# Performance work log

Hardware: AMD Instinct MI355X
Metric: run time of the kernel (lower is better)

## Reference

```python
import jax, jax.numpy as jnp
import numpy as np
from jax.scipy.special import digamma, gammaln

B, N, H, W, D = 16, 1024, 32, 32, 256
TEMP = 0.5
KL_WEIGHT = 1e-3


def setup_inputs() -> dict:
    key = jax.random.key(0)
    k1, k2, k3 = jax.random.split(key, 3)
    logits = jax.random.normal(k1, (B, N, H, W), dtype=jnp.float32)
    # codebook initialized uniform(-1/N, 1/N) as in init_type == 'uniform'
    codebook = jax.random.uniform(k2, (N, D), dtype=jnp.float32,
                                  minval=-1.0 / N, maxval=1.0 / N)
    # uniform noise for the Gumbel-softmax rsample (channels-last layout [B,H,W,N])
    uniform_noise = jax.random.uniform(k3, (B, H, W, N), dtype=jnp.float32,
                                       minval=1e-6, maxval=1.0 - 1e-6)
    return {"logits": logits, "codebook": codebook, "uniform_noise": uniform_noise}


def reference(logits, codebook, uniform_noise):
    # convert_to_alpha: evidential mapping alpha = softplus(logits) + 1,
    # then permute(0,2,3,1) -> [B, H, W, N]
    alpha = jax.nn.softplus(jnp.transpose(logits, (0, 2, 3, 1))) + 1.0
    S = jnp.sum(alpha, axis=-1, keepdims=True)            # [B,H,W,1]
    probs = alpha / S                                      # [B,H,W,N]

    # RelaxedOneHotCategorical(temp, probs).rsample() == Gumbel-softmax
    gumbel = -jnp.log(-jnp.log(uniform_noise))
    sample = jax.nn.softmax((jnp.log(probs) + gumbel) / TEMP, axis=-1)  # [B,H,W,N]

    vector_weights = jnp.transpose(sample, (0, 3, 1, 2))   # [B,N,H,W]
    indices = jnp.argmax(vector_weights, axis=1)           # [B,H,W]

    # quantized output via codebook combine
    z_q = jnp.einsum('bnhw,nd->bdhw', vector_weights, codebook)  # [B,D,H,W]

    # KL( Dirichlet(alpha) || Dirichlet(ones(N)) ), closed form with beta=1:
    # lgamma(S) - sum lgamma(alpha) - lgamma(N) + sum (alpha-1)*(digamma(alpha)-digamma(S))
    S1 = S[..., 0]
    kl = (gammaln(S1)
          - jnp.sum(gammaln(alpha), axis=-1)
          - gammaln(jnp.float32(N))
          + jnp.sum((alpha - 1.0) * (digamma(alpha) - digamma(S)), axis=-1))
    kl_loss = KL_WEIGHT * jnp.mean(kl)

    # perplexity over soft encodings
    avg_probs = jnp.mean(sample.reshape(-1, N), axis=0)
    perplexity = jnp.exp(-jnp.sum(avg_probs * jnp.log(avg_probs + 1e-10)))

    return (z_q, kl_loss, indices, perplexity)
```

## Files before the change

### kernel.cpp

```cpp
#include <hip/hip_runtime.h>
#include <math.h>

#define NB 16
#define NN 1024
#define NH 32
#define NW 32
#define ND 256
#define NPIX (NB*NH*NW)

#define ZQ_OFF  0
#define KL_OFF  4194304
#define IDX_OFF 4194305
#define PPL_OFF 4210689

#define LGAMMA_1024F 6071.2804f
#define BS_ROW_B 2080

typedef _Float16 f16x8 __attribute__((ext_vector_type(8)));
typedef _Float16 f16x4 __attribute__((ext_vector_type(4)));
typedef float    f32x4 __attribute__((ext_vector_type(4)));

__device__ __forceinline__ float fast_rcp(float x){ return __builtin_amdgcn_rcpf(x); }

__device__ __forceinline__ void lgamma_digamma(float a, float& lg, float& dg){
    float a1 = a + 1.f, a2 = a + 2.f, z = a + 3.f;
    float t12  = a1*a2;
    float prod = a*t12;
    float rz = fast_rcp(z);
    float rp = fast_rcp(prod);
    float lz = __logf(z);
    float lp = __logf(prod);
    float rz2 = rz*rz;
    lg = (z - 0.5f)*lz - z + 0.918938533f
       + rz*(0.083333333f - 0.002777778f*rz2) - lp;
    float sr = (t12 + a*(a + a + 3.f))*rp;
    dg = lz - 0.5f*rz - rz2*(0.083333333f - 0.008333333f*rz2) - sr;
}

__device__ __forceinline__ float elem(float x, float u,
                                      float& S, float& L, float& P){
    float t  = __expf(-fabsf(x));
    float a  = fmaxf(x, 0.f) + __logf(1.f + t) + 1.f;
    float lg, dg;
    lgamma_digamma(a, lg, dg);
    S += a; L += lg; P += (a - 1.f)*dg;
    float d = 1.f - u;
    float lup = -d*(1.f + d*(0.5f + d*(0.33333333f + d*(0.25f
              + d*(0.2f + d*(0.16666667f + d*0.14285714f))))));
    float lu = (d < 0.09f) ? lup : __logf(u);
    float ar = a * fast_rcp(lu);
    return ar*ar;
}

__global__ __launch_bounds__(256) void k_tr(
    const float* __restrict__ cb, _Float16* __restrict__ cbT)
{
    const int kb = blockIdx.x, kq = blockIdx.y, d = threadIdx.x;
    _Float16 tmp[8];
#pragma unroll
    for (int i = 0; i < 8; ++i)
        tmp[i] = (_Float16)cb[(size_t)(32*kb + 8*kq + i)*ND + d];
    *(f16x8*)(cbT + (size_t)kb*8192 + (size_t)d*32 + 8*kq) = *(f16x8*)tmp;
}

__global__ __launch_bounds__(1024, 2) void k_mega(
    const float* __restrict__ logits, const float* __restrict__ noise,
    const _Float16* __restrict__ cbT, float* __restrict__ colpart,
    float* __restrict__ klpart, float* __restrict__ out)
{
    __shared__ __align__(16) char lds[16*BS_ROW_B + 6*256*4];
    char*  bsb  = lds;
    float* redS = (float*)(lds + 16*BS_ROW_B);
    float* redL = redS + 256;
    float* redP = redL + 256;
    float* redZ = redP + 256;
    float* redM = redZ + 256;
    int*   redI = (int*)(redM + 256);

    const int t    = threadIdx.x;
    const int row  = blockIdx.x >> 1;
    const int w0   = (blockIdx.x & 1) * 16;
    const int b    = row >> 5, h = row & 31;
    const int lane = t & 63;
    const int v    = t >> 6;
    const int wl   = lane & 15;
    const int j4   = (lane >> 4) & 3;
    const int p    = row*32 + w0 + wl;
    const int nq   = 4*v + j4;

    const float* lgB = logits + (size_t)b*(NN*NH*NW) + (size_t)(4*nq)*(NH*NW)
                     + (size_t)h*NW + w0 + wl;
    const float* nzB = noise  + (size_t)p*NN + 4*nq;

    f32x4 u0, u1, u2, u3;
    float x00,x01,x02,x03, x10,x11,x12,x13;
    float x20,x21,x22,x23, x30,x31,x32,x33;
    float ev[16];
    float Sa = 0.f, La = 0.f, Pa = 0.f, Za = 0.f;
    float Sb = 0.f, Lb = 0.f, Pb = 0.f, Zb = 0.f;
    float mxA = -1.f, mxB = -1.f;
    int   idxA = 0, idxB = 0;

    asm volatile(
        "global_load_dwordx4 %0, %4, off\n\t"
        "global_load_dwordx4 %1, %4, off offset:1024\n\t"
        "global_load_dwordx4 %2, %4, off offset:2048\n\t"
        "global_load_dwordx4 %3, %4, off offset:3072"
        : "=&v"(u0), "=&v"(u1), "=&v"(u2), "=&v"(u3)
        : "v"(nzB));

#define LG_ASM(X0,X1,X2,X3,KK) \
    asm volatile( \
        "global_load_dword %0, %4, off offset:-4096\n\t" \
        "global_load_dword %1, %4, off\n\t" \
        "global_load_dword %2, %5, off offset:-4096\n\t" \
        "global_load_dword %3, %5, off" \
        : "=&v"(X0), "=&v"(X1), "=&v"(X2), "=&v"(X3) \
        : "v"(lgB + (size_t)(256*(KK))*1024 + 1024), \
          "v"(lgB + (size_t)(256*(KK))*1024 + 3072))

    LG_ASM(x00,x01,x02,x03, 0);
    LG_ASM(x10,x11,x12,x13, 1);
    LG_ASM(x20,x21,x22,x23, 2);
    LG_ASM(x30,x31,x32,x33, 3);
#undef LG_ASM

#define WAITV(NSTR) do{ asm volatile("s_waitcnt vmcnt(" NSTR ")"); \
                        __builtin_amdgcn_sched_barrier(0); }while(0)

#define DO_EA(kk,mm,X,UC) do{                                     \
    float e = elem(X, UC, Sa, La, Pa);                            \
    Za += e;                                                      \
    if (e > mxA){ mxA = e; idxA = 256*(kk) + 4*nq + (mm); }       \
    ev[4*(kk)+(mm)] = e; }while(0)

#define DO_EB(kk,mm,X,UC) do{                                     \
    float e = elem(X, UC, Sb, Lb, Pb);                            \
    Zb += e;                                                      \
    if (e > mxB){ mxB = e; idxB = 256*(kk) + 4*nq + (mm); }       \
    ev[4*(kk)+(mm)] = e; }while(0)

    WAITV("12");
    DO_EA(0,0,x00,u0[0]); DO_EB(0,1,x01,u0[1]);
    DO_EA(0,2,x02,u0[2]); DO_EB(0,3,x03,u0[3]);
    WAITV("8");
    DO_EA(1,0,x10,u1[0]); DO_EB(1,1,x11,u1[1]);
    DO_EA(1,2,x12,u1[2]); DO_EB(1,3,x13,u1[3]);
    WAITV("4");
    DO_EA(2,0,x20,u2[0]); DO_EB(2,1,x21,u2[1]);
    DO_EA(2,2,x22,u2[2]); DO_EB(2,3,x23,u2[3]);
    WAITV("0");
    DO_EA(3,0,x30,u3[0]); DO_EB(3,1,x31,u3[1]);
    DO_EA(3,2,x32,u3[2]); DO_EB(3,3,x33,u3[3]);
#undef WAITV
#undef DO_EA
#undef DO_EB

    float S = Sa + Sb, L = La + Lb, P = Pa + Pb, Z = Za + Zb;
    float mx; int idx;
    {
        bool take = (mxB > mxA) || (mxB == mxA && idxB < idxA);
        mx  = take ? mxB : mxA;
        idx = take ? idxB : idxA;
    }

#pragma unroll
    for (int mask = 16; mask < 64; mask <<= 1){
        S += __shfl_xor(S, mask);
        L += __shfl_xor(L, mask);
        P += __shfl_xor(P, mask);
        Z += __shfl_xor(Z, mask);
        float mo = __shfl_xor(mx, mask);
        int   io = __shfl_xor(idx, mask);
        bool take = (mo > mx) || (mo == mx && io < idx);
        mx  = take ? mo : mx;
        idx = take ? io : idx;
    }
    if (j4 == 0){
        redS[16*v + wl] = S;  redL[16*v + wl] = L;
        redP[16*v + wl] = P;  redZ[16*v + wl] = Z;
        redM[16*v + wl] = mx; redI[16*v + wl] = idx;
    }
    __syncthreads();

    float Zt = 0.f;
#pragma unroll
    for (int qz = 0; qz < 16; ++qz) Zt += redZ[16*qz + wl];
    const float zinv = fast_rcp(Zt);

    {
        char* brow = bsb + wl*BS_ROW_B;
        const int sw   = wl & 7;
        const int sub8 = (nq & 1) << 3;
        const int cb2  = nq >> 1;
#pragma unroll
        for (int k = 0; k < 4; ++k){
            f16x4 hv;
            hv[0] = (_Float16)(ev[4*k+0]*zinv);
            hv[1] = (_Float16)(ev[4*k+1]*zinv);
            hv[2] = (_Float16)(ev[4*k+2]*zinv);
            hv[3] = (_Float16)(ev[4*k+3]*zinv);
            *(f16x4*)(brow + (((32*k + cb2) ^ sw) << 4) + sub8) = hv;
        }
    }
    __syncthreads();

    const _Float16* aBase = cbT + (size_t)(16*v + wl)*32 + j4*8;
    const char* bRow = bsb + wl*BS_ROW_B;
    const int fsw = wl & 7;

    f32x4 acc = (f32x4)0.f;
    f16x8 ar[4];
    ar[0] = *(const f16x8*)(aBase);
    ar[1] = *(const f16x8*)(aBase + 8192);
    ar[2] = *(const f16x8*)(aBase + 2*8192);
    __builtin_amdgcn_sched_barrier(0);

#pragma unroll
    for (int kb = 0; kb < 32; ++kb){
        if (kb + 3 < 32){
            ar[(kb+3)&3] = *(const f16x8*)(aBase + (size_t)(kb+3)*8192);
            __builtin_amdgcn_sched_barrier(0);
        }
        f16x8 bf = *(const f16x8*)(bRow + ((((kb << 2) | j4) ^ fsw) << 4));
        acc = __builtin_amdgcn_mfma_f32_16x16x32_f16(ar[kb&3], bf, acc, 0, 0, 0);
    }

    float* outp = out + (size_t)b*(ND*1024) + h*32 + w0;
#pragma unroll
    for (int r = 0; r < 4; ++r){
        int d = 16*v + 4*j4 + r;
        outp[(size_t)d*1024 + wl] = acc[r];
    }

    {
        float s0 = 0.f;
#pragma unroll
        for (int r = 0; r < 16; ++r){
            const char* br = bsb + r*BS_ROW_B;
            const int sw2 = r & 7;
            s0 += (float)*(const _Float16*)(br + ((((t >> 3) ^ sw2) << 4) + 2*(t & 7)));
        }
        colpart[(size_t)blockIdx.x*NN + t] = s0;
    }

    if (t < 16){
        float Sq = 0.f, Lq = 0.f, Pq = 0.f, M = -1.f;
        int I = 0x7fffffff;
#pragma unroll
        for (int qz = 0; qz < 16; ++qz){
            Sq += redS[16*qz + t]; Lq += redL[16*qz + t]; Pq += redP[16*qz + t];
            float m = redM[16*qz + t]; int i = redI[16*qz + t];
            bool take = (m > M) || (m == M && i < I);
            M = take ? m : M; I = take ? i : I;
        }
        out[IDX_OFF + row*32 + w0 + t] = (float)I;
        float rS  = fast_rcp(Sq);
        float lnS = __logf(Sq);
        float lgS = (Sq - 0.5f)*lnS - Sq + 0.918938533f + 0.083333333f*rS;
        float dgS = lnS - 0.5f*rS;
        float kl = lgS - Lq - LGAMMA_1024F + (Pq - dgS*(Sq - 1024.f));
#pragma unroll
        for (int mask = 1; mask < 16; mask <<= 1) kl += __shfl_xor(kl, mask);
        if (t == 0) klpart[blockIdx.x] = kl;
    }
}

__global__ __launch_bounds__(256) void k_red(
    const float* __restrict__ colpart, float* __restrict__ colsum)
{
    __shared__ float red[8][32];
    const int nl = threadIdx.x & 31;
    const int rs = threadIdx.x >> 5;
    const int n  = blockIdx.x*32 + nl;
    const float* cp = colpart + (size_t)rs*128*NN + n;
    float s = 0.f;
#pragma unroll 8
    for (int r = 0; r < 128; ++r)
        s += cp[(size_t)r*NN];
    red[rs][nl] = s;
    __syncthreads();
    if (threadIdx.x < 32){
        float tot = 0.f;
#pragma unroll
        for (int i = 0; i < 8; ++i) tot += red[i][threadIdx.x];
        colsum[blockIdx.x*32 + threadIdx.x] = tot;
    }
}

__global__ __launch_bounds__(256) void k_final(
    const float* __restrict__ colsum, const float* __restrict__ klpart,
    float* __restrict__ out)
{
    __shared__ float red[8];
    const int tid = threadIdx.x;
    float s = 0.f, kls = 0.f;
#pragma unroll
    for (int n = tid; n < NN; n += 256){
        float avg = colsum[n] * (1.f/16384.f);
        s += avg * logf(avg + 1e-10f);
        kls += klpart[n];
    }
#pragma unroll
    for (int mask = 1; mask < 64; mask <<= 1){
        s   += __shfl_xor(s, mask);
        kls += __shfl_xor(kls, mask);
    }
    if ((tid & 63) == 0){ red[tid >> 6] = s; red[4 + (tid >> 6)] = kls; }
    __syncthreads();
    if (tid == 0){
        float tot = red[0] + red[1] + red[2] + red[3];
        float klt = red[4] + red[5] + red[6] + red[7];
        out[PPL_OFF] = expf(-tot);
        out[KL_OFF]  = 1e-3f * (klt * (1.f/16384.f));
    }
}

extern "C" void kernel_launch(void* const* d_in, const int* in_sizes, int n_in,
                              void* d_out, int out_size, void* d_ws, size_t ws_size,
                              hipStream_t stream)
{
    const float* logits = (const float*)d_in[0];
    const float* cb     = (const float*)d_in[1];
    const float* noise  = (const float*)d_in[2];
    float* out = (float*)d_out;

    float* colpart = (float*)d_ws;
    float* colsum  = colpart + (size_t)1024*NN;
    float* klpart  = colsum + NN;
    _Float16* cbT  = (_Float16*)(klpart + NN);

    k_tr   <<<dim3(32, 4), 256, 0, stream>>>(cb, cbT);
    k_mega <<<dim3(1024), 1024, 0, stream>>>(logits, noise, cbT, colpart, klpart, out);
    k_red  <<<dim3(32),    256, 0, stream>>>(colpart, colsum);
    k_final<<<1, 256, 0, stream>>>(colsum, klpart, out);
}
```

Measured before the change: 204.5 us.

## Pack element math into float2 vectors and defer lgamma product logs

Rewrites the per-element softplus/lgamma/digamma computation on two-wide float vectors so the compiler can emit packed FP32 instructions. It also drops the per-element log(prod) term from lgamma: the products are multiplied into running accumulators and a single log is taken per accumulator at the end. Separately, it removes the sched_barriers around the codebook prefetch in the MFMA loop, letting the compiler schedule loads freely. This trades transcendental work for a risk of overflow or precision loss when multiplying eight products of values up to around 3x, and it may change how well load latency is hidden.

```diff
diff --git a/kernel.cpp b/kernel.cpp
--- a/kernel.cpp
+++ b/kernel.cpp
@@ -19,36 +19,37 @@
 typedef _Float16 f16x8 __attribute__((ext_vector_type(8)));
 typedef _Float16 f16x4 __attribute__((ext_vector_type(4)));
 typedef float    f32x4 __attribute__((ext_vector_type(4)));
+typedef float    f32x2 __attribute__((ext_vector_type(2)));
 
 __device__ __forceinline__ float fast_rcp(float x){ return __builtin_amdgcn_rcpf(x); }
 
-__device__ __forceinline__ void lgamma_digamma(float a, float& lg, float& dg){
-    float a1 = a + 1.f, a2 = a + 2.f, z = a + 3.f;
-    float t12  = a1*a2;
-    float prod = a*t12;
-    float rz = fast_rcp(z);
-    float rp = fast_rcp(prod);
-    float lz = __logf(z);
-    float lp = __logf(prod);
-    float rz2 = rz*rz;
-    lg = (z - 0.5f)*lz - z + 0.918938533f
-       + rz*(0.083333333f - 0.002777778f*rz2) - lp;
-    float sr = (t12 + a*(a + a + 3.f))*rp;
-    dg = lz - 0.5f*rz - rz2*(0.083333333f - 0.008333333f*rz2) - sr;
-}
-
-__device__ __forceinline__ float elem(float x, float u,
-                                      float& S, float& L, float& P){
-    float t  = __expf(-fabsf(x));
-    float a  = fmaxf(x, 0.f) + __logf(1.f + t) + 1.f;
-    float lg, dg;
-    lgamma_digamma(a, lg, dg);
+__device__ __forceinline__ f32x2 elem2(f32x2 x, f32x2 u,
+                                       f32x2& S, f32x2& L, f32x2& P,
+                                       f32x2& prodAcc){
+    f32x2 t;   t[0] = __expf(-fabsf(x[0]));  t[1] = __expf(-fabsf(x[1]));
+    f32x2 mx0; mx0[0] = fmaxf(x[0], 0.f);    mx0[1] = fmaxf(x[1], 0.f);
+    f32x2 l1p; l1p[0] = __logf(1.f + t[0]);  l1p[1] = __logf(1.f + t[1]);
+    f32x2 a  = mx0 + l1p + 1.f;
+    f32x2 a1 = a + 1.f, a2 = a + 2.f, z = a + 3.f;
+    f32x2 t12  = a1*a2;
+    f32x2 prod = a*t12;
+    f32x2 rz;  rz[0] = fast_rcp(z[0]);       rz[1] = fast_rcp(z[1]);
+    f32x2 rp;  rp[0] = fast_rcp(prod[0]);    rp[1] = fast_rcp(prod[1]);
+    f32x2 lz;  lz[0] = __logf(z[0]);         lz[1] = __logf(z[1]);
+    prodAcc = prodAcc * prod;
+    f32x2 rz2 = rz*rz;
+    f32x2 lg = (z - 0.5f)*lz - z + 0.918938533f
+             + rz*(0.083333333f - 0.002777778f*rz2);
+    f32x2 sr = (t12 + a*(a + a + 3.f))*rp;
+    f32x2 dg = lz - 0.5f*rz - rz2*(0.083333333f - 0.008333333f*rz2) - sr;
     S += a; L += lg; P += (a - 1.f)*dg;
-    float d = 1.f - u;
-    float lup = -d*(1.f + d*(0.5f + d*(0.33333333f + d*(0.25f
+    f32x2 d = 1.f - u;
+    f32x2 lup = -d*(1.f + d*(0.5f + d*(0.33333333f + d*(0.25f
               + d*(0.2f + d*(0.16666667f + d*0.14285714f))))));
-    float lu = (d < 0.09f) ? lup : __logf(u);
-    float ar = a * fast_rcp(lu);
+    f32x2 lu;
+    lu[0] = (d[0] < 0.09f) ? lup[0] : __logf(u[0]);
+    lu[1] = (d[1] < 0.09f) ? lup[1] : __logf(u[1]);
+    f32x2 ar; ar[0] = a[0]*fast_rcp(lu[0]);  ar[1] = a[1]*fast_rcp(lu[1]);
     return ar*ar;
 }
 
@@ -96,8 +97,9 @@
     float x00,x01,x02,x03, x10,x11,x12,x13;
     float x20,x21,x22,x23, x30,x31,x32,x33;
     float ev[16];
-    float Sa = 0.f, La = 0.f, Pa = 0.f, Za = 0.f;
-    float Sb = 0.f, Lb = 0.f, Pb = 0.f, Zb = 0.f;
+    f32x2 SA = (f32x2)0.f, LA = (f32x2)0.f, PA = (f32x2)0.f, ZA = (f32x2)0.f;
+    f32x2 SB = (f32x2)0.f, LB = (f32x2)0.f, PB = (f32x2)0.f, ZB = (f32x2)0.f;
+    f32x2 prA = (f32x2)1.f, prB = (f32x2)1.f;
     float mxA = -1.f, mxB = -1.f;
     int   idxA = 0, idxB = 0;
 
@@ -128,35 +130,36 @@
 #define WAITV(NSTR) do{ asm volatile("s_waitcnt vmcnt(" NSTR ")"); \
                         __builtin_amdgcn_sched_barrier(0); }while(0)
 
-#define DO_EA(kk,mm,X,UC) do{                                     \
-    float e = elem(X, UC, Sa, La, Pa);                            \
-    Za += e;                                                      \
-    if (e > mxA){ mxA = e; idxA = 256*(kk) + 4*nq + (mm); }       \
-    ev[4*(kk)+(mm)] = e; }while(0)
-
-#define DO_EB(kk,mm,X,UC) do{                                     \
-    float e = elem(X, UC, Sb, Lb, Pb);                            \
-    Zb += e;                                                      \
-    if (e > mxB){ mxB = e; idxB = 256*(kk) + 4*nq + (mm); }       \
-    ev[4*(kk)+(mm)] = e; }while(0)
+#define DO_PAIR(kk, X0,X1,X2,X3, UV) do{                          \
+    f32x2 xA_, xB_, uA_, uB_;                                     \
+    xA_[0]=X0; xA_[1]=X1; xB_[0]=X2; xB_[1]=X3;                   \
+    uA_[0]=UV[0]; uA_[1]=UV[1]; uB_[0]=UV[2]; uB_[1]=UV[3];       \
+    f32x2 eA = elem2(xA_, uA_, SA, LA, PA, prA);                  \
+    f32x2 eB = elem2(xB_, uB_, SB, LB, PB, prB);                  \
+    ZA += eA; ZB += eB;                                           \
+    if (eA[0] > mxA){ mxA = eA[0]; idxA = 256*(kk) + 4*nq + 0; }  \
+    if (eA[1] > mxA){ mxA = eA[1]; idxA = 256*(kk) + 4*nq + 1; }  \
+    if (eB[0] > mxB){ mxB = eB[0]; idxB = 256*(kk) + 4*nq + 2; }  \
+    if (eB[1] > mxB){ mxB = eB[1]; idxB = 256*(kk) + 4*nq + 3; }  \
+    ev[4*(kk)+0]=eA[0]; ev[4*(kk)+1]=eA[1];                       \
+    ev[4*(kk)+2]=eB[0]; ev[4*(kk)+3]=eB[1]; }while(0)
 
     WAITV("12");
-    DO_EA(0,0,x00,u0[0]); DO_EB(0,1,x01,u0[1]);
-    DO_EA(0,2,x02,u0[2]); DO_EB(0,3,x03,u0[3]);
+    DO_PAIR(0, x00,x01,x02,x03, u0);
     WAITV("8");
-    DO_EA(1,0,x10,u1[0]); DO_EB(1,1,x11,u1[1]);
-    DO_EA(1,2,x12,u1[2]); DO_EB(1,3,x13,u1[3]);
+    DO_PAIR(1, x10,x11,x12,x13, u1);
     WAITV("4");
-    DO_EA(2,0,x20,u2[0]); DO_EB(2,1,x21,u2[1]);
-    DO_EA(2,2,x22,u2[2]); DO_EB(2,3,x23,u2[3]);
+    DO_PAIR(2, x20,x21,x22,x23, u2);
     WAITV("0");
-    DO_EA(3,0,x30,u3[0]); DO_EB(3,1,x31,u3[1]);
-    DO_EA(3,2,x32,u3[2]); DO_EB(3,3,x33,u3[3]);
+    DO_PAIR(3, x30,x31,x32,x33, u3);
 #undef WAITV
-#undef DO_EA
-#undef DO_EB
-
-    float S = Sa + Sb, L = La + Lb, P = Pa + Pb, Z = Za + Zb;
+#undef DO_PAIR
+
+    float S = (SA[0] + SA[1]) + (SB[0] + SB[1]);
+    float L = (LA[0] + LA[1]) + (LB[0] + LB[1])
+            - __logf(prA[0]*prA[1]) - __logf(prB[0]*prB[1]);
+    float P = (PA[0] + PA[1]) + (PB[0] + PB[1]);
+    float Z = (ZA[0] + ZA[1]) + (ZB[0] + ZB[1]);
     float mx; int idx;
     {
         bool take = (mxB > mxA) || (mxB == mxA && idxB < idxA);
@@ -214,14 +217,11 @@
     ar[0] = *(const f16x8*)(aBase);
     ar[1] = *(const f16x8*)(aBase + 8192);
     ar[2] = *(const f16x8*)(aBase + 2*8192);
-    __builtin_amdgcn_sched_barrier(0);
 
 #pragma unroll
     for (int kb = 0; kb < 32; ++kb){
-        if (kb + 3 < 32){
+        if (kb + 3 < 32)
             ar[(kb+3)&3] = *(const f16x8*)(aBase + (size_t)(kb+3)*8192);
-            __builtin_amdgcn_sched_barrier(0);
-        }
         f16x8 bf = *(const f16x8*)(bRow + ((((kb << 2) | j4) ^ fsw) << 4));
         acc = __builtin_amdgcn_mfma_f32_16x16x32_f16(ar[kb&3], bf, acc, 0, 0, 0);
     }
```

Result: slower. 214.0 us (+4.7%).
